# Kernel optimization log

Measured on AMD Instinct MI355X. Metric: run time of the kernel, lower is better.

Reference implementation:

```python
import jax, jax.numpy as jnp
from jax import lax
import numpy as np

IN, HID, NCLS, B, S = 360, 64, 5, 64, 128
MH_CONST = 2.0 / (np.sqrt(3.0) * np.pi ** 0.25)


def setup_inputs() -> dict:
    key = jax.random.key(0)
    ks = jax.random.split(key, 24)
    g = lambda i, shape, s=0.05: jax.random.normal(ks[i], shape, jnp.float32) * s
    inp = {
        'x_seq': jax.random.normal(ks[0], (B, S, IN), jnp.float32),
        # WavKANLinear params (out=64, in=360)
        'wav_scale': jnp.ones((HID, IN), jnp.float32),
        'wav_translation': jnp.zeros((HID, IN), jnp.float32),
        'wav_weights': g(1, (HID, IN)),
        'base_weight': g(2, (HID, IN)),
        # BatchNorm1d (eval mode, running stats)
        'bn_gamma': jnp.ones((HID,), jnp.float32),
        'bn_beta': jnp.zeros((HID,), jnp.float32),
        'bn_mean': jnp.zeros((HID,), jnp.float32),
        'bn_var': jnp.ones((HID,), jnp.float32),
        # LayerNorm(64)
        'ln_gamma': jnp.ones((HID,), jnp.float32),
        'ln_beta': jnp.zeros((HID,), jnp.float32),
        # bidirectional GRU, 1 layer, hidden=64
        'gru_w_ih_f': g(3, (3 * HID, HID)), 'gru_w_hh_f': g(4, (3 * HID, HID)),
        'gru_b_ih_f': g(5, (3 * HID,)), 'gru_b_hh_f': g(6, (3 * HID,)),
        'gru_w_ih_b': g(7, (3 * HID, HID)), 'gru_w_hh_b': g(8, (3 * HID, HID)),
        'gru_b_ih_b': g(9, (3 * HID,)), 'gru_b_hh_b': g(10, (3 * HID,)),
        # classifier: Linear(128,64) -> ReLU -> Linear(64,5)
        'fc1_w': g(11, (HID, 2 * HID)), 'fc1_b': jnp.zeros((HID,), jnp.float32),
        'fc2_w': g(12, (NCLS, HID)), 'fc2_b': jnp.zeros((NCLS,), jnp.float32),
    }
    return inp


def _gru_dir(x_sbf, w_ih, w_hh, b_ih, b_hh, reverse):
    # x_sbf: (S, B, F). Returns final hidden (B, H). PyTorch GRU equations.
    Bn = x_sbf.shape[1]
    H = w_hh.shape[1]
    gi_all = jnp.einsum('sbf,gf->sbg', x_sbf, w_ih) + b_ih  # precompute input gates

    def step(h, gi):
        gh = h @ w_hh.T + b_hh
        i_r, i_z, i_n = jnp.split(gi, 3, axis=-1)
        h_r, h_z, h_n = jnp.split(gh, 3, axis=-1)
        r = jax.nn.sigmoid(i_r + h_r)
        z = jax.nn.sigmoid(i_z + h_z)
        n = jnp.tanh(i_n + r * h_n)
        h_new = (1.0 - z) * n + z * h
        return h_new, None

    h0 = jnp.zeros((Bn, H), x_sbf.dtype)
    h_final, _ = lax.scan(step, h0, gi_all, reverse=reverse)
    return h_final


def reference(x_seq, wav_scale, wav_translation, wav_weights, base_weight,
              bn_gamma, bn_beta, bn_mean, bn_var, ln_gamma, ln_beta,
              gru_w_ih_f, gru_w_hh_f, gru_b_ih_f, gru_b_hh_f,
              gru_w_ih_b, gru_w_hh_b, gru_b_ih_b, gru_b_hh_b,
              fc1_w, fc1_b, fc2_w, fc2_b):
    b, s, f = x_seq.shape
    x_flat = x_seq.reshape(b * s, f)  # (N, 360)

    # --- WavKANLinear (mexican_hat) ---
    x_scaled = (x_flat[:, None, :] - wav_translation[None]) / wav_scale[None]  # (N, 64, 360)
    wavelet = MH_CONST * (x_scaled * x_scaled - 1.0) * jnp.exp(-0.5 * x_scaled * x_scaled)
    wav_out = jnp.einsum('noi,oi->no', wavelet, wav_weights)  # (N, 64)
    base_out = jax.nn.silu(x_flat) @ base_weight.T
    combined = wav_out + base_out
    # BatchNorm1d eval mode
    x_emb = (combined - bn_mean) * lax.rsqrt(bn_var + 1e-5) * bn_gamma + bn_beta

    # --- LayerNorm(64) ---
    mu = jnp.mean(x_emb, axis=-1, keepdims=True)
    var = jnp.mean(jnp.square(x_emb - mu), axis=-1, keepdims=True)
    x_emb = (x_emb - mu) * lax.rsqrt(var + 1e-5) * ln_gamma + ln_beta
    # dropout is identity in eval mode

    x_sbf = x_emb.reshape(b, s, HID).swapaxes(0, 1)  # (S, B, 64)

    # --- bidirectional GRU, take final hiddens ---
    h_fwd = _gru_dir(x_sbf, gru_w_ih_f, gru_w_hh_f, gru_b_ih_f, gru_b_hh_f, False)
    h_bwd = _gru_dir(x_sbf, gru_w_ih_b, gru_w_hh_b, gru_b_ih_b, gru_b_hh_b, True)
    hidden_cat = jnp.concatenate([h_fwd, h_bwd], axis=1)  # (B, 128)

    # --- classifier ---
    h = jax.nn.relu(hidden_cat @ fc1_w.T + fc1_b)
    logits = h @ fc2_w.T + fc2_b
    return logits
```

## Files before the change

### kernel.cpp

```cpp
#include <hip/hip_runtime.h>

#define IN_F   360
#define HIDN   64
#define NCLS   5
#define BATCH  64
#define SEQ    128
#define NROWS  (BATCH*SEQ)

#define WS_FLAG  0
#define WS_WPACK 16
#define WS_WFAST 92176
#define WS_WT4   138256
#define WS_XEMB  162832
#define WS_GI    687120
#define WS_HC    3832848

#define LOG2E        1.4426950408889634f
#define NEG_HALF_L2E (-0.7213475204444817f)

__device__ __forceinline__ float fast_rcp(float x) { return __builtin_amdgcn_rcpf(x); }
__device__ __forceinline__ float fast_rsq(float x) { return __builtin_amdgcn_rsqf(x); }
__device__ __forceinline__ float sigmoid_(float x) {
    x = fminf(fmaxf(x, -60.0f), 60.0f);
    return fast_rcp(1.0f + exp2f(-LOG2E * x));
}
__device__ __forceinline__ float tanh_(float x) {
    x = fminf(fmaxf(x, -30.0f), 30.0f);
    float e = exp2f(-2.8853900817779268f * x);
    return (1.0f - e) * fast_rcp(1.0f + e);
}
__device__ __forceinline__ float readlane_f(float v, int l) {
    return __int_as_float(__builtin_amdgcn_readlane(__float_as_int(v), l));
}

__global__ __launch_bounds__(256) void prep_kernel(
    const float* __restrict__ scale, const float* __restrict__ trans,
    const float* __restrict__ ww,    const float* __restrict__ bw,
    const float* __restrict__ wihf,  const float* __restrict__ wihb,
    float* __restrict__ ws) {
    int idx = blockIdx.x * 256 + threadIdx.x;
    float4* wpack  = (float4*)(ws + WS_WPACK);
    float2* wfast2 = (float2*)(ws + WS_WFAST);
    float*  wT4    = ws + WS_WT4;
    int*    flagp  = (int*)(ws + WS_FLAG);
    if (idx < 64 * IN_F) {
        int o = idx & 63, i = idx >> 6;
        float s  = scale[o * IN_F + i];
        float tr = trans[o * IN_F + i];
        if (s != 1.0f || tr != 0.0f) atomicOr(flagp, 1);
        float a  = 1.0f / s;
        float b  = -tr * a;
        float wq = 0.8673250705840776f * ww[o * IN_F + i];
        float bb = bw[o * IN_F + i];
        wpack[i * 64 + o] = make_float4(a, b, wq, bb);
        wfast2[(i >> 1) * 128 + o * 2 + (i & 1)] = make_float2(wq, bb);
    }
    int idx2 = idx - 64 * IN_F;
    if (idx2 >= 0 && idx2 < 24576) {
        int e = idx2 & 3; int rest = idx2 >> 2;
        int g = rest % 384; int k4 = rest / 384;
        int k = k4 * 4 + e; int dir = g / 192; int gg = g - dir * 192;
        const float* src = dir ? wihb : wihf;
        wT4[idx2] = src[gg * 64 + k];
    }
}

__global__ __launch_bounds__(512) void wavgi_kernel(
    const float* __restrict__ x_seq,
    const float* __restrict__ bn_g, const float* __restrict__ bn_b,
    const float* __restrict__ bn_m, const float* __restrict__ bn_v,
    const float* __restrict__ ln_g, const float* __restrict__ ln_b,
    const float* __restrict__ ws_c,
    const float* __restrict__ bihf, const float* __restrict__ bihb,
    float* __restrict__ gi) {
    __shared__ float2 xs_lds[16 * IN_F];
    __shared__ __align__(16) float xs2[32 * 64];
    int t = threadIdx.x;
    int row0 = blockIdx.x * 32;
    int o = t & 63, grp = t >> 6;
    int fast = (*(const int*)(ws_c + WS_FLAG)) == 0;

    float bscale = bn_g[o] * fast_rsq(bn_v[o] + 1e-5f);
    float bshift = fmaf(-bn_m[o], bscale, bn_b[o]);
    float lg = ln_g[o], lb = ln_b[o];

    for (int st = 0; st < 2; ++st) {
        if (st) __syncthreads();
        float acc0 = 0.f, acc1 = 0.f;
        if (fast) {
            for (int idx = t; idx < 16 * IN_F; idx += 512) {
                int r = idx / IN_F, i = idx - r * IN_F;
                float x = x_seq[(row0 + st * 16 + r) * IN_F + i];
                float u = x * x;
                float phi = (u - 1.0f) * exp2f(u * NEG_HALF_L2E);
                float sl  = x * fast_rcp(1.0f + exp2f(-LOG2E * x));
                xs_lds[idx] = make_float2(phi, sl);
            }
            __syncthreads();
            const float4* wf4 = (const float4*)(ws_c + WS_WFAST);
            const float4* xs4 = (const float4*)xs_lds;
            const float4* xr0 = xs4 + (grp * 2 + 0) * 180;
            const float4* xr1 = xs4 + (grp * 2 + 1) * 180;
            #pragma unroll 2
            for (int i2 = 0; i2 < 180; ++i2) {
                float4 wp = wf4[i2 * 64 + o];
                float4 a = xr0[i2];
                acc0 = fmaf(a.x, wp.x, acc0); acc0 = fmaf(a.y, wp.y, acc0);
                acc0 = fmaf(a.z, wp.z, acc0); acc0 = fmaf(a.w, wp.w, acc0);
                float4 b = xr1[i2];
                acc1 = fmaf(b.x, wp.x, acc1); acc1 = fmaf(b.y, wp.y, acc1);
                acc1 = fmaf(b.z, wp.z, acc1); acc1 = fmaf(b.w, wp.w, acc1);
            }
        } else {
            for (int idx = t; idx < 16 * IN_F; idx += 512) {
                int r = idx / IN_F, i = idx - r * IN_F;
                float x = x_seq[(row0 + st * 16 + r) * IN_F + i];
                float sl = x * fast_rcp(1.0f + exp2f(-LOG2E * x));
                xs_lds[idx] = make_float2(x, sl);
            }
            __syncthreads();
            const float4* wpack = (const float4*)(ws_c + WS_WPACK);
            const float2* xr0 = xs_lds + (grp * 2 + 0) * IN_F;
            const float2* xr1 = xs_lds + (grp * 2 + 1) * IN_F;
            for (int i = 0; i < IN_F; ++i) {
                float4 wp = wpack[i * 64 + o];
                {
                    float2 xs = xr0[i];
                    float xsc = fmaf(xs.x, wp.x, wp.y); float u = xsc * xsc;
                    float e = exp2f(u * NEG_HALF_L2E);
                    acc0 = fmaf((u - 1.0f) * e, wp.z, acc0);
                    acc0 = fmaf(xs.y, wp.w, acc0);
                }
                {
                    float2 xs = xr1[i];
                    float xsc = fmaf(xs.x, wp.x, wp.y); float u = xsc * xsc;
                    float e = exp2f(u * NEG_HALF_L2E);
                    acc1 = fmaf((u - 1.0f) * e, wp.z, acc1);
                    acc1 = fmaf(xs.y, wp.w, acc1);
                }
            }
        }
        float vals[2] = {acc0, acc1};
        #pragma unroll
        for (int rr = 0; rr < 2; ++rr) {
            float y = fmaf(vals[rr], bscale, bshift);
            float s = y;
            #pragma unroll
            for (int m = 1; m < 64; m <<= 1) s += __shfl_xor(s, m, 64);
            float mu = s * (1.0f / 64.0f);
            float d = y - mu;
            float s2 = d * d;
            #pragma unroll
            for (int m = 1; m < 64; m <<= 1) s2 += __shfl_xor(s2, m, 64);
            float rstd = fast_rsq(s2 * (1.0f / 64.0f) + 1e-5f);
            xs2[(st * 16 + grp * 2 + rr) * 64 + o] = fmaf(d * rstd, lg, lb);
        }
    }
    __syncthreads();

    if (t < 384) {
        const float4* wT4 = (const float4*)(ws_c + WS_WT4);
        int dir = t / 192, gg = t - dir * 192;
        float bih = dir ? bihb[gg] : bihf[gg];
        float4 w[16];
        #pragma unroll
        for (int k4 = 0; k4 < 16; ++k4) w[k4] = wT4[k4 * 384 + t];
        for (int r = 0; r < 32; r += 2) {
            const float4* x0 = (const float4*)(xs2 + r * 64);
            const float4* x1 = (const float4*)(xs2 + r * 64 + 64);
            float a0 = bih, a1 = 0.f, b0 = bih, b1 = 0.f;
            #pragma unroll
            for (int k4 = 0; k4 < 16; k4 += 2) {
                float4 xv = x0[k4];     float4 wv = w[k4];
                a0 = fmaf(xv.x, wv.x, a0); a0 = fmaf(xv.y, wv.y, a0);
                a0 = fmaf(xv.z, wv.z, a0); a0 = fmaf(xv.w, wv.w, a0);
                float4 xu = x0[k4 + 1]; float4 wu = w[k4 + 1];
                a1 = fmaf(xu.x, wu.x, a1); a1 = fmaf(xu.y, wu.y, a1);
                a1 = fmaf(xu.z, wu.z, a1); a1 = fmaf(xu.w, wu.w, a1);
                float4 yv = x1[k4];
                b0 = fmaf(yv.x, wv.x, b0); b0 = fmaf(yv.y, wv.y, b0);
                b0 = fmaf(yv.z, wv.z, b0); b0 = fmaf(yv.w, wv.w, b0);
                float4 yu = x1[k4 + 1];
                b1 = fmaf(yu.x, wu.x, b1); b1 = fmaf(yu.y, wu.y, b1);
                b1 = fmaf(yu.z, wu.z, b1); b1 = fmaf(yu.w, wu.w, b1);
            }
            gi[(row0 + r) * 384 + t]     = a0 + a1;
            gi[(row0 + r + 1) * 384 + t] = b0 + b1;
        }
    }
}

__global__ __launch_bounds__(192, 1) void gru_kernel(
    const float* __restrict__ ws_c,
    const float* __restrict__ whhf, const float* __restrict__ bhhf,
    const float* __restrict__ whhb, const float* __restrict__ bhhb,
    float* __restrict__ hc) {
    __shared__ __align__(16) float gi_l[64 * 192];
    __shared__ __align__(16) float ex[2][192];
    const float* gi = ws_c + WS_GI;
    int t = threadIdx.x, lane = t & 63, g = t >> 6;
    int b = blockIdx.x & 63, dir = blockIdx.x >> 6;
    const float* whh = dir ? whhb : whhf;
    const float* bhh = dir ? bhhb : bhhf;

    float w[64];
    {
        const float4* wrow = (const float4*)(whh + t * 64);
        #pragma unroll
        for (int q = 0; q < 16; ++q) {
            float4 a = wrow[q];
            w[4*q] = a.x; w[4*q+1] = a.y; w[4*q+2] = a.z; w[4*q+3] = a.w;
        }
    }
    float bias = bhh[t];

    const float* gsrc = gi + (size_t)(b * SEQ) * 384 + dir * 192 + t;
#define GOFF(s) ((dir ? (SEQ - 1 - (s)) : (s)) * 384)
    #pragma unroll 8
    for (int q = 0; q < 64; ++q) gi_l[q * 192 + t] = gsrc[GOFF(q)];
    float h = 0.0f;
    __syncthreads();

    for (int ss = 0; ss < SEQ; ++ss) {
        if (ss == 64) {
            __syncthreads();
            #pragma unroll 8
            for (int q = 0; q < 64; ++q) gi_l[q * 192 + t] = gsrc[GOFF(64 + q)];
            __syncthreads();
        }
        int ssl = ss & 63, p = ss & 1;
        float giv = gi_l[ssl * 192 + t];
        float inv = gi_l[ssl * 192 + 128 + lane];
        float acc0 = bias, acc1 = 0.f;
        #pragma unroll
        for (int c = 0; c < 4; ++c) {
            float sh[16];
            #pragma unroll
            for (int j = 0; j < 16; ++j) sh[j] = readlane_f(h, c * 16 + j);
            #pragma unroll
            for (int j = 0; j < 16; j += 2) {
                acc0 = fmaf(w[c * 16 + j],     sh[j],     acc0);
                acc1 = fmaf(w[c * 16 + j + 1], sh[j + 1], acc1);
            }
        }
        float a = acc0 + acc1;
        float v = (g == 2) ? a : sigmoid_(giv + a);
        ex[p][t] = v;
        __syncthreads();
        float r   = ex[p][lane];
        float z   = ex[p][64 + lane];
        float an  = ex[p][128 + lane];
        float n = tanh_(fmaf(r, an, inv));
        h = fmaf(z, h - n, n);
    }
#undef GOFF
    if (g == 0) hc[b * 128 + dir * 64 + lane] = h;
}

__global__ __launch_bounds__(64) void head_kernel(
    const float* __restrict__ ws_c,
    const float* __restrict__ fc1w, const float* __restrict__ fc1b,
    const float* __restrict__ fc2w, const float* __restrict__ fc2b,
    float* __restrict__ out) {
    __shared__ __align__(16) float hr[128];
    __shared__ float h1[64];
    const float* hc = ws_c + WS_HC;
    int bb = blockIdx.x, t = threadIdx.x;
    hr[t]      = hc[bb * 128 + t];
    hr[64 + t] = hc[bb * 128 + 64 + t];
    __syncthreads();
    float acc = fc1b[t];
    const float4* w4 = (const float4*)(fc1w + t * 128);
    const float4* h4 = (const float4*)hr;
    #pragma unroll 8
    for (int k4 = 0; k4 < 32; ++k4) {
        float4 wv = w4[k4]; float4 hv = h4[k4];
        acc = fmaf(hv.x, wv.x, acc); acc = fmaf(hv.y, wv.y, acc);
        acc = fmaf(hv.z, wv.z, acc); acc = fmaf(hv.w, wv.w, acc);
    }
    h1[t] = fmaxf(acc, 0.0f);
    __syncthreads();
    if (t < NCLS) {
        float acc2 = fc2b[t];
        const float* wr = fc2w + t * 64;
        #pragma unroll 8
        for (int k = 0; k < 64; ++k) acc2 = fmaf(h1[k], wr[k], acc2);
        out[bb * NCLS + t] = acc2;
    }
}

extern "C" void kernel_launch(void* const* d_in, const int* in_sizes, int n_in,
                              void* d_out, int out_size, void* d_ws, size_t ws_size,
                              hipStream_t stream) {
    const float* x_seq = (const float*)d_in[0];
    const float* wscal = (const float*)d_in[1];
    const float* wtran = (const float*)d_in[2];
    const float* wwght = (const float*)d_in[3];
    const float* bwght = (const float*)d_in[4];
    const float* bn_g  = (const float*)d_in[5];
    const float* bn_b  = (const float*)d_in[6];
    const float* bn_m  = (const float*)d_in[7];
    const float* bn_v  = (const float*)d_in[8];
    const float* ln_g  = (const float*)d_in[9];
    const float* ln_b  = (const float*)d_in[10];
    const float* wihf  = (const float*)d_in[11];
    const float* whhf  = (const float*)d_in[12];
    const float* bihf  = (const float*)d_in[13];
    const float* bhhf  = (const float*)d_in[14];
    const float* wihb  = (const float*)d_in[15];
    const float* whhb  = (const float*)d_in[16];
    const float* bihb  = (const float*)d_in[17];
    const float* bhhb  = (const float*)d_in[18];
    const float* fc1w  = (const float*)d_in[19];
    const float* fc1b  = (const float*)d_in[20];
    const float* fc2w  = (const float*)d_in[21];
    const float* fc2b  = (const float*)d_in[22];
    float* ws  = (float*)d_ws;
    float* out = (float*)d_out;

    hipMemsetAsync(ws + WS_FLAG, 0, sizeof(int), stream);
    hipLaunchKernelGGL(prep_kernel, dim3(186), dim3(256), 0, stream,
                       wscal, wtran, wwght, bwght, wihf, wihb, ws);
    hipLaunchKernelGGL(wavgi_kernel, dim3(NROWS / 32), dim3(512), 0, stream,
                       x_seq, bn_g, bn_b, bn_m, bn_v, ln_g, ln_b, ws,
                       bihf, bihb, ws + WS_GI);
    hipLaunchKernelGGL(gru_kernel, dim3(128), dim3(192), 0, stream,
                       ws, whhf, bhhf, whhb, bhhb, ws + WS_HC);
    hipLaunchKernelGGL(head_kernel, dim3(64), dim3(64), 0, stream,
                       ws, fc1w, fc1b, fc2w, fc2b, out);
}
```

Before: 240.8 us.

## Fuse all stages into one cooperative kernel with grid syncs

Merges the prep, wavelet/gate-precompute, GRU recurrence and classifier-head kernels into a single cooperative launch of 256 blocks, separated by grid-wide barriers. A shared-memory union is reused across stages. The input-gate GEMM loop is also restructured to stream weights once while keeping 32 row accumulators in registers. The aim is to remove per-launch overhead between the four kernels. In exchange, the GRU stage now runs with 512-thread blocks at one block per CU where only 192 threads are active, grid.sync has its own cost, and register pressure rises.

```diff
diff --git a/kernel.cpp b/kernel.cpp
--- a/kernel.cpp
+++ b/kernel.cpp
@@ -1,4 +1,7 @@
 #include <hip/hip_runtime.h>
+#include <hip/hip_cooperative_groups.h>
+
+namespace cg = cooperative_groups;
 
 #define IN_F   360
 #define HIDN   64
@@ -33,259 +36,268 @@
     return __int_as_float(__builtin_amdgcn_readlane(__float_as_int(v), l));
 }
 
-__global__ __launch_bounds__(256) void prep_kernel(
+__global__ __launch_bounds__(512, 1) void mega_kernel(
+    const float* __restrict__ x_seq,
     const float* __restrict__ scale, const float* __restrict__ trans,
     const float* __restrict__ ww,    const float* __restrict__ bw,
+    const float* __restrict__ bn_g,  const float* __restrict__ bn_b,
+    const float* __restrict__ bn_m,  const float* __restrict__ bn_v,
+    const float* __restrict__ ln_g,  const float* __restrict__ ln_b,
     const float* __restrict__ wihf,  const float* __restrict__ wihb,
-    float* __restrict__ ws) {
-    int idx = blockIdx.x * 256 + threadIdx.x;
-    float4* wpack  = (float4*)(ws + WS_WPACK);
-    float2* wfast2 = (float2*)(ws + WS_WFAST);
-    float*  wT4    = ws + WS_WT4;
-    int*    flagp  = (int*)(ws + WS_FLAG);
-    if (idx < 64 * IN_F) {
-        int o = idx & 63, i = idx >> 6;
-        float s  = scale[o * IN_F + i];
-        float tr = trans[o * IN_F + i];
-        if (s != 1.0f || tr != 0.0f) atomicOr(flagp, 1);
-        float a  = 1.0f / s;
-        float b  = -tr * a;
-        float wq = 0.8673250705840776f * ww[o * IN_F + i];
-        float bb = bw[o * IN_F + i];
-        wpack[i * 64 + o] = make_float4(a, b, wq, bb);
-        wfast2[(i >> 1) * 128 + o * 2 + (i & 1)] = make_float2(wq, bb);
+    const float* __restrict__ bihf,  const float* __restrict__ bihb,
+    const float* __restrict__ whhf,  const float* __restrict__ bhhf,
+    const float* __restrict__ whhb,  const float* __restrict__ bhhb,
+    const float* __restrict__ fc1w,  const float* __restrict__ fc1b,
+    const float* __restrict__ fc2w,  const float* __restrict__ fc2b,
+    float* __restrict__ ws, float* __restrict__ out) {
+
+    __shared__ __align__(16) union SM {
+        struct { float2 xs[16 * IN_F]; float xs2[32 * 64]; } s12;
+        struct { float gi_l[64 * 192]; float ex[2][192]; } s3;
+        struct { float hr[128]; float h1[64]; } s4;
+    } sm;
+
+    cg::grid_group grid = cg::this_grid();
+    int t = threadIdx.x, bid = blockIdx.x;
+    float* gi = ws + WS_GI;
+    float* hc = ws + WS_HC;
+
+    {
+        int idx = bid * 512 + t;
+        float4* wpack  = (float4*)(ws + WS_WPACK);
+        float2* wfast2 = (float2*)(ws + WS_WFAST);
+        float*  wT4    = ws + WS_WT4;
+        int*    flagp  = (int*)(ws + WS_FLAG);
+        if (idx < 64 * IN_F) {
+            int o = idx & 63, i = idx >> 6;
+            float s  = scale[o * IN_F + i];
+            float tr = trans[o * IN_F + i];
+            if (s != 1.0f || tr != 0.0f) atomicOr(flagp, 1);
+            float a  = 1.0f / s;
+            float b  = -tr * a;
+            float wq = 0.8673250705840776f * ww[o * IN_F + i];
+            float bb = bw[o * IN_F + i];
+            wpack[i * 64 + o] = make_float4(a, b, wq, bb);
+            wfast2[(i >> 1) * 128 + o * 2 + (i & 1)] = make_float2(wq, bb);
+        }
+        int idx2 = idx - 64 * IN_F;
+        if (idx2 >= 0 && idx2 < 24576) {
+            int e = idx2 & 3; int rest = idx2 >> 2;
+            int g = rest % 384; int k4 = rest / 384;
+            int k = k4 * 4 + e; int dir = g / 192; int gg = g - dir * 192;
+            const float* src = dir ? wihb : wihf;
+            wT4[idx2] = src[gg * 64 + k];
+        }
     }
-    int idx2 = idx - 64 * IN_F;
-    if (idx2 >= 0 && idx2 < 24576) {
-        int e = idx2 & 3; int rest = idx2 >> 2;
-        int g = rest % 384; int k4 = rest / 384;
-        int k = k4 * 4 + e; int dir = g / 192; int gg = g - dir * 192;
-        const float* src = dir ? wihb : wihf;
-        wT4[idx2] = src[gg * 64 + k];
+    __threadfence();
+    grid.sync();
+    __threadfence();
+
+    {
+        int row0 = bid * 32;
+        int o = t & 63, grp = t >> 6;
+        int fast = (*(const int*)(ws + WS_FLAG)) == 0;
+        float bscale = bn_g[o] * fast_rsq(bn_v[o] + 1e-5f);
+        float bshift = fmaf(-bn_m[o], bscale, bn_b[o]);
+        float lg = ln_g[o], lb = ln_b[o];
+
+        for (int st = 0; st < 2; ++st) {
+            if (st) __syncthreads();
+            float acc0 = 0.f, acc1 = 0.f;
+            if (fast) {
+                for (int idx = t; idx < 16 * IN_F; idx += 512) {
+                    int r = idx / IN_F, i = idx - r * IN_F;
+                    float x = x_seq[(row0 + st * 16 + r) * IN_F + i];
+                    float u = x * x;
+                    float phi = (u - 1.0f) * exp2f(u * NEG_HALF_L2E);
+                    float sl  = x * fast_rcp(1.0f + exp2f(-LOG2E * x));
+                    sm.s12.xs[idx] = make_float2(phi, sl);
+                }
+                __syncthreads();
+                const float4* wf4 = (const float4*)(ws + WS_WFAST);
+                const float4* xs4 = (const float4*)sm.s12.xs;
+                const float4* xr0 = xs4 + (grp * 2 + 0) * 180;
+                const float4* xr1 = xs4 + (grp * 2 + 1) * 180;
+                #pragma unroll 2
+                for (int i2 = 0; i2 < 180; ++i2) {
+                    float4 wp = wf4[i2 * 64 + o];
+                    float4 a = xr0[i2];
+                    acc0 = fmaf(a.x, wp.x, acc0); acc0 = fmaf(a.y, wp.y, acc0);
+                    acc0 = fmaf(a.z, wp.z, acc0); acc0 = fmaf(a.w, wp.w, acc0);
+                    float4 b = xr1[i2];
+                    acc1 = fmaf(b.x, wp.x, acc1); acc1 = fmaf(b.y, wp.y, acc1);
+                    acc1 = fmaf(b.z, wp.z, acc1); acc1 = fmaf(b.w, wp.w, acc1);
+                }
+            } else {
+                for (int idx = t; idx < 16 * IN_F; idx += 512) {
+                    int r = idx / IN_F, i = idx - r * IN_F;
+                    float x = x_seq[(row0 + st * 16 + r) * IN_F + i];
+                    float sl = x * fast_rcp(1.0f + exp2f(-LOG2E * x));
+                    sm.s12.xs[idx] = make_float2(x, sl);
+                }
+                __syncthreads();
+                const float4* wpack = (const float4*)(ws + WS_WPACK);
+                const float2* xr0 = sm.s12.xs + (grp * 2 + 0) * IN_F;
+                const float2* xr1 = sm.s12.xs + (grp * 2 + 1) * IN_F;
+                for (int i = 0; i < IN_F; ++i) {
+                    float4 wp = wpack[i * 64 + o];
+                    {
+                        float2 xsv = xr0[i];
+                        float xsc = fmaf(xsv.x, wp.x, wp.y); float u = xsc * xsc;
+                        float e = exp2f(u * NEG_HALF_L2E);
+                        acc0 = fmaf((u - 1.0f) * e, wp.z, acc0);
+                        acc0 = fmaf(xsv.y, wp.w, acc0);
+                    }
+                    {
+                        float2 xsv = xr1[i];
+                        float xsc = fmaf(xsv.x, wp.x, wp.y); float u = xsc * xsc;
+                        float e = exp2f(u * NEG_HALF_L2E);
+                        acc1 = fmaf((u - 1.0f) * e, wp.z, acc1);
+                        acc1 = fmaf(xsv.y, wp.w, acc1);
+                    }
+                }
+            }
+            float vals[2] = {acc0, acc1};
+            #pragma unroll
+            for (int rr = 0; rr < 2; ++rr) {
+                float y = fmaf(vals[rr], bscale, bshift);
+                float s = y;
+                #pragma unroll
+                for (int m = 1; m < 64; m <<= 1) s += __shfl_xor(s, m, 64);
+                float mu = s * (1.0f / 64.0f);
+                float d = y - mu;
+                float s2 = d * d;
+                #pragma unroll
+                for (int m = 1; m < 64; m <<= 1) s2 += __shfl_xor(s2, m, 64);
+                float rstd = fast_rsq(s2 * (1.0f / 64.0f) + 1e-5f);
+                sm.s12.xs2[(st * 16 + grp * 2 + rr) * 64 + o] = fmaf(d * rstd, lg, lb);
+            }
+        }
+        __syncthreads();
+
+        if (t < 384) {
+            const float4* wT4 = (const float4*)(ws + WS_WT4);
+            int dir = t / 192, gg = t - dir * 192;
+            float bih = dir ? bihb[gg] : bihf[gg];
+            float acc[32];
+            #pragma unroll
+            for (int j = 0; j < 32; ++j) acc[j] = bih;
+            const float4* x4 = (const float4*)sm.s12.xs2;
+            for (int k4 = 0; k4 < 16; ++k4) {
+                float4 wv = wT4[k4 * 384 + t];
+                #pragma unroll
+                for (int j = 0; j < 32; ++j) {
+                    float4 xv = x4[j * 16 + k4];
+                    acc[j] = fmaf(xv.x, wv.x, acc[j]);
+                    acc[j] = fmaf(xv.y, wv.y, acc[j]);
+                    acc[j] = fmaf(xv.z, wv.z, acc[j]);
+                    acc[j] = fmaf(xv.w, wv.w, acc[j]);
+                }
+            }
+            #pragma unroll
+            for (int j = 0; j < 32; ++j) gi[(size_t)(row0 + j) * 384 + t] = acc[j];
+        }
     }
-}
-
-__global__ __launch_bounds__(512) void wavgi_kernel(
-    const float* __restrict__ x_seq,
-    const float* __restrict__ bn_g, const float* __restrict__ bn_b,
-    const float* __restrict__ bn_m, const float* __restrict__ bn_v,
-    const float* __restrict__ ln_g, const float* __restrict__ ln_b,
-    const float* __restrict__ ws_c,
-    const float* __restrict__ bihf, const float* __restrict__ bihb,
-    float* __restrict__ gi) {
-    __shared__ float2 xs_lds[16 * IN_F];
-    __shared__ __align__(16) float xs2[32 * 64];
-    int t = threadIdx.x;
-    int row0 = blockIdx.x * 32;
-    int o = t & 63, grp = t >> 6;
-    int fast = (*(const int*)(ws_c + WS_FLAG)) == 0;
-
-    float bscale = bn_g[o] * fast_rsq(bn_v[o] + 1e-5f);
-    float bshift = fmaf(-bn_m[o], bscale, bn_b[o]);
-    float lg = ln_g[o], lb = ln_b[o];
-
-    for (int st = 0; st < 2; ++st) {
-        if (st) __syncthreads();
-        float acc0 = 0.f, acc1 = 0.f;
-        if (fast) {
-            for (int idx = t; idx < 16 * IN_F; idx += 512) {
-                int r = idx / IN_F, i = idx - r * IN_F;
-                float x = x_seq[(row0 + st * 16 + r) * IN_F + i];
-                float u = x * x;
-                float phi = (u - 1.0f) * exp2f(u * NEG_HALF_L2E);
-                float sl  = x * fast_rcp(1.0f + exp2f(-LOG2E * x));
-                xs_lds[idx] = make_float2(phi, sl);
+    __threadfence();
+    grid.sync();
+    __threadfence();
+
+    if (bid < 128) {
+        int lane = t & 63, g = t >> 6;
+        bool act = t < 192;
+        int b = bid & 63, dirg = bid >> 6;
+        const float* whh = dirg ? whhb : whhf;
+        const float* bhh = dirg ? bhhb : bhhf;
+        float w[64];
+        float bias = 0.f, h = 0.f;
+        const float* gsrc = gi + (size_t)(b * SEQ) * 384 + dirg * 192 + t;
+#define GOFF(s) ((dirg ? (SEQ - 1 - (s)) : (s)) * 384)
+        if (act) {
+            const float4* wrow = (const float4*)(whh + t * 64);
+            #pragma unroll
+            for (int q = 0; q < 16; ++q) {
+                float4 a = wrow[q];
+                w[4*q] = a.x; w[4*q+1] = a.y; w[4*q+2] = a.z; w[4*q+3] = a.w;
+            }
+            bias = bhh[t];
+            #pragma unroll 8
+            for (int q = 0; q < 64; ++q) sm.s3.gi_l[q * 192 + t] = gsrc[GOFF(q)];
+        }
+        __syncthreads();
+
+        for (int ss = 0; ss < SEQ; ++ss) {
+            if (ss == 64) {
+                __syncthreads();
+                if (act) {
+                    #pragma unroll 8
+                    for (int q = 0; q < 64; ++q)
+                        sm.s3.gi_l[q * 192 + t] = gsrc[GOFF(64 + q)];
+                }
+                __syncthreads();
+            }
+            int ssl = ss & 63, p = ss & 1;
+            float inv = 0.f;
+            if (act) {
+                float giv = sm.s3.gi_l[ssl * 192 + t];
+                inv       = sm.s3.gi_l[ssl * 192 + 128 + lane];
+                float acc0 = bias, acc1 = 0.f;
+                #pragma unroll
+                for (int c = 0; c < 4; ++c) {
+                    float sh[16];
+                    #pragma unroll
+                    for (int j = 0; j < 16; ++j) sh[j] = readlane_f(h, c * 16 + j);
+                    #pragma unroll
+                    for (int j = 0; j < 16; j += 2) {
+                        acc0 = fmaf(w[c * 16 + j],     sh[j],     acc0);
+                        acc1 = fmaf(w[c * 16 + j + 1], sh[j + 1], acc1);
+                    }
+                }
+                float a = acc0 + acc1;
+                float v = (g == 2) ? a : sigmoid_(giv + a);
+                sm.s3.ex[p][t] = v;
             }
             __syncthreads();
-            const float4* wf4 = (const float4*)(ws_c + WS_WFAST);
-            const float4* xs4 = (const float4*)xs_lds;
-            const float4* xr0 = xs4 + (grp * 2 + 0) * 180;
-            const float4* xr1 = xs4 + (grp * 2 + 1) * 180;
-            #pragma unroll 2
-            for (int i2 = 0; i2 < 180; ++i2) {
-                float4 wp = wf4[i2 * 64 + o];
-                float4 a = xr0[i2];
-                acc0 = fmaf(a.x, wp.x, acc0); acc0 = fmaf(a.y, wp.y, acc0);
-                acc0 = fmaf(a.z, wp.z, acc0); acc0 = fmaf(a.w, wp.w, acc0);
-                float4 b = xr1[i2];
-                acc1 = fmaf(b.x, wp.x, acc1); acc1 = fmaf(b.y, wp.y, acc1);
-                acc1 = fmaf(b.z, wp.z, acc1); acc1 = fmaf(b.w, wp.w, acc1);
-            }
-        } else {
-            for (int idx = t; idx < 16 * IN_F; idx += 512) {
-                int r = idx / IN_F, i = idx - r * IN_F;
-                float x = x_seq[(row0 + st * 16 + r) * IN_F + i];
-                float sl = x * fast_rcp(1.0f + exp2f(-LOG2E * x));
-                xs_lds[idx] = make_float2(x, sl);
-            }
-            __syncthreads();
-            const float4* wpack = (const float4*)(ws_c + WS_WPACK);
-            const float2* xr0 = xs_lds + (grp * 2 + 0) * IN_F;
-            const float2* xr1 = xs_lds + (grp * 2 + 1) * IN_F;
-            for (int i = 0; i < IN_F; ++i) {
-                float4 wp = wpack[i * 64 + o];
-                {
-                    float2 xs = xr0[i];
-                    float xsc = fmaf(xs.x, wp.x, wp.y); float u = xsc * xsc;
-                    float e = exp2f(u * NEG_HALF_L2E);
-                    acc0 = fmaf((u - 1.0f) * e, wp.z, acc0);
-                    acc0 = fmaf(xs.y, wp.w, acc0);
-                }
-                {
-                    float2 xs = xr1[i];
-                    float xsc = fmaf(xs.x, wp.x, wp.y); float u = xsc * xsc;
-                    float e = exp2f(u * NEG_HALF_L2E);
-                    acc1 = fmaf((u - 1.0f) * e, wp.z, acc1);
-                    acc1 = fmaf(xs.y, wp.w, acc1);
-                }
-            }
-        }
-        float vals[2] = {acc0, acc1};
-        #pragma unroll
-        for (int rr = 0; rr < 2; ++rr) {
-            float y = fmaf(vals[rr], bscale, bshift);
-            float s = y;
-            #pragma unroll
-            for (int m = 1; m < 64; m <<= 1) s += __shfl_xor(s, m, 64);
-            float mu = s * (1.0f / 64.0f);
-            float d = y - mu;
-            float s2 = d * d;
-            #pragma unroll
-            for (int m = 1; m < 64; m <<= 1) s2 += __shfl_xor(s2, m, 64);
-            float rstd = fast_rsq(s2 * (1.0f / 64.0f) + 1e-5f);
-            xs2[(st * 16 + grp * 2 + rr) * 64 + o] = fmaf(d * rstd, lg, lb);
-        }
+            if (act) {
+                float r  = sm.s3.ex[p][lane];
+                float z  = sm.s3.ex[p][64 + lane];
+                float an = sm.s3.ex[p][128 + lane];
+                float n = tanh_(fmaf(r, an, inv));
+                h = fmaf(z, h - n, n);
+            }
+        }
+#undef GOFF
+        if (act && g == 0) hc[b * 128 + dirg * 64 + lane] = h;
     }
-    __syncthreads();
-
-    if (t < 384) {
-        const float4* wT4 = (const float4*)(ws_c + WS_WT4);
-        int dir = t / 192, gg = t - dir * 192;
-        float bih = dir ? bihb[gg] : bihf[gg];
-        float4 w[16];
-        #pragma unroll
-        for (int k4 = 0; k4 < 16; ++k4) w[k4] = wT4[k4 * 384 + t];
-        for (int r = 0; r < 32; r += 2) {
-            const float4* x0 = (const float4*)(xs2 + r * 64);
-            const float4* x1 = (const float4*)(xs2 + r * 64 + 64);
-            float a0 = bih, a1 = 0.f, b0 = bih, b1 = 0.f;
-            #pragma unroll
-            for (int k4 = 0; k4 < 16; k4 += 2) {
-                float4 xv = x0[k4];     float4 wv = w[k4];
-                a0 = fmaf(xv.x, wv.x, a0); a0 = fmaf(xv.y, wv.y, a0);
-                a0 = fmaf(xv.z, wv.z, a0); a0 = fmaf(xv.w, wv.w, a0);
-                float4 xu = x0[k4 + 1]; float4 wu = w[k4 + 1];
-                a1 = fmaf(xu.x, wu.x, a1); a1 = fmaf(xu.y, wu.y, a1);
-                a1 = fmaf(xu.z, wu.z, a1); a1 = fmaf(xu.w, wu.w, a1);
-                float4 yv = x1[k4];
-                b0 = fmaf(yv.x, wv.x, b0); b0 = fmaf(yv.y, wv.y, b0);
-                b0 = fmaf(yv.z, wv.z, b0); b0 = fmaf(yv.w, wv.w, b0);
-                float4 yu = x1[k4 + 1];
-                b1 = fmaf(yu.x, wu.x, b1); b1 = fmaf(yu.y, wu.y, b1);
-                b1 = fmaf(yu.z, wu.z, b1); b1 = fmaf(yu.w, wu.w, b1);
-            }
-            gi[(row0 + r) * 384 + t]     = a0 + a1;
-            gi[(row0 + r + 1) * 384 + t] = b0 + b1;
-        }
-    }
-}
-
-__global__ __launch_bounds__(192, 1) void gru_kernel(
-    const float* __restrict__ ws_c,
-    const float* __restrict__ whhf, const float* __restrict__ bhhf,
-    const float* __restrict__ whhb, const float* __restrict__ bhhb,
-    float* __restrict__ hc) {
-    __shared__ __align__(16) float gi_l[64 * 192];
-    __shared__ __align__(16) float ex[2][192];
-    const float* gi = ws_c + WS_GI;
-    int t = threadIdx.x, lane = t & 63, g = t >> 6;
-    int b = blockIdx.x & 63, dir = blockIdx.x >> 6;
-    const float* whh = dir ? whhb : whhf;
-    const float* bhh = dir ? bhhb : bhhf;
-
-    float w[64];
-    {
-        const float4* wrow = (const float4*)(whh + t * 64);
-        #pragma unroll
-        for (int q = 0; q < 16; ++q) {
-            float4 a = wrow[q];
-            w[4*q] = a.x; w[4*q+1] = a.y; w[4*q+2] = a.z; w[4*q+3] = a.w;
-        }
-    }
-    float bias = bhh[t];
-
-    const float* gsrc = gi + (size_t)(b * SEQ) * 384 + dir * 192 + t;
-#define GOFF(s) ((dir ? (SEQ - 1 - (s)) : (s)) * 384)
-    #pragma unroll 8
-    for (int q = 0; q < 64; ++q) gi_l[q * 192 + t] = gsrc[GOFF(q)];
-    float h = 0.0f;
-    __syncthreads();
-
-    for (int ss = 0; ss < SEQ; ++ss) {
-        if (ss == 64) {
-            __syncthreads();
+    __threadfence();
+    grid.sync();
+    __threadfence();
+
+    if (bid < 64) {
+        if (t < 64) {
+            sm.s4.hr[t]      = hc[bid * 128 + t];
+            sm.s4.hr[64 + t] = hc[bid * 128 + 64 + t];
+        }
+        __syncthreads();
+        if (t < 64) {
+            float acc = fc1b[t];
+            const float4* w4 = (const float4*)(fc1w + t * 128);
+            const float4* h4 = (const float4*)sm.s4.hr;
             #pragma unroll 8
-            for (int q = 0; q < 64; ++q) gi_l[q * 192 + t] = gsrc[GOFF(64 + q)];
-            __syncthreads();
-        }
-        int ssl = ss & 63, p = ss & 1;
-        float giv = gi_l[ssl * 192 + t];
-        float inv = gi_l[ssl * 192 + 128 + lane];
-        float acc0 = bias, acc1 = 0.f;
-        #pragma unroll
-        for (int c = 0; c < 4; ++c) {
-            float sh[16];
-            #pragma unroll
-            for (int j = 0; j < 16; ++j) sh[j] = readlane_f(h, c * 16 + j);
-            #pragma unroll
-            for (int j = 0; j < 16; j += 2) {
-                acc0 = fmaf(w[c * 16 + j],     sh[j],     acc0);
-                acc1 = fmaf(w[c * 16 + j + 1], sh[j + 1], acc1);
-            }
-        }
-        float a = acc0 + acc1;
-        float v = (g == 2) ? a : sigmoid_(giv + a);
-        ex[p][t] = v;
+            for (int k4 = 0; k4 < 32; ++k4) {
+                float4 wv = w4[k4]; float4 hv = h4[k4];
+                acc = fmaf(hv.x, wv.x, acc); acc = fmaf(hv.y, wv.y, acc);
+                acc = fmaf(hv.z, wv.z, acc); acc = fmaf(hv.w, wv.w, acc);
+            }
+            sm.s4.h1[t] = fmaxf(acc, 0.0f);
+        }
         __syncthreads();
-        float r   = ex[p][lane];
-        float z   = ex[p][64 + lane];
-        float an  = ex[p][128 + lane];
-        float n = tanh_(fmaf(r, an, inv));
-        h = fmaf(z, h - n, n);
-    }
-#undef GOFF
-    if (g == 0) hc[b * 128 + dir * 64 + lane] = h;
-}
-
-__global__ __launch_bounds__(64) void head_kernel(
-    const float* __restrict__ ws_c,
-    const float* __restrict__ fc1w, const float* __restrict__ fc1b,
-    const float* __restrict__ fc2w, const float* __restrict__ fc2b,
-    float* __restrict__ out) {
-    __shared__ __align__(16) float hr[128];
-    __shared__ float h1[64];
-    const float* hc = ws_c + WS_HC;
-    int bb = blockIdx.x, t = threadIdx.x;
-    hr[t]      = hc[bb * 128 + t];
-    hr[64 + t] = hc[bb * 128 + 64 + t];
-    __syncthreads();
-    float acc = fc1b[t];
-    const float4* w4 = (const float4*)(fc1w + t * 128);
-    const float4* h4 = (const float4*)hr;
-    #pragma unroll 8
-    for (int k4 = 0; k4 < 32; ++k4) {
-        float4 wv = w4[k4]; float4 hv = h4[k4];
-        acc = fmaf(hv.x, wv.x, acc); acc = fmaf(hv.y, wv.y, acc);
-        acc = fmaf(hv.z, wv.z, acc); acc = fmaf(hv.w, wv.w, acc);
-    }
-    h1[t] = fmaxf(acc, 0.0f);
-    __syncthreads();
-    if (t < NCLS) {
-        float acc2 = fc2b[t];
-        const float* wr = fc2w + t * 64;
-        #pragma unroll 8
-        for (int k = 0; k < 64; ++k) acc2 = fmaf(h1[k], wr[k], acc2);
-        out[bb * NCLS + t] = acc2;
+        if (t < NCLS) {
+            float acc2 = fc2b[t];
+            const float* wr = fc2w + t * 64;
+            #pragma unroll 8
+            for (int k = 0; k < 64; ++k) acc2 = fmaf(sm.s4.h1[k], wr[k], acc2);
+            out[bid * NCLS + t] = acc2;
+        }
     }
 }
 
@@ -319,13 +331,15 @@
     float* out = (float*)d_out;
 
     hipMemsetAsync(ws + WS_FLAG, 0, sizeof(int), stream);
-    hipLaunchKernelGGL(prep_kernel, dim3(186), dim3(256), 0, stream,
-                       wscal, wtran, wwght, bwght, wihf, wihb, ws);
-    hipLaunchKernelGGL(wavgi_kernel, dim3(NROWS / 32), dim3(512), 0, stream,
-                       x_seq, bn_g, bn_b, bn_m, bn_v, ln_g, ln_b, ws,
-                       bihf, bihb, ws + WS_GI);
-    hipLaunchKernelGGL(gru_kernel, dim3(128), dim3(192), 0, stream,
-                       ws, whhf, bhhf, whhb, bhhb, ws + WS_HC);
-    hipLaunchKernelGGL(head_kernel, dim3(64), dim3(64), 0, stream,
-                       ws, fc1w, fc1b, fc2w, fc2b, out);
-}
+    void* args[] = {
+        (void*)&x_seq, (void*)&wscal, (void*)&wtran, (void*)&wwght, (void*)&bwght,
+        (void*)&bn_g, (void*)&bn_b, (void*)&bn_m, (void*)&bn_v,
+        (void*)&ln_g, (void*)&ln_b,
+        (void*)&wihf, (void*)&wihb, (void*)&bihf, (void*)&bihb,
+        (void*)&whhf, (void*)&bhhf, (void*)&whhb, (void*)&bhhb,
+        (void*)&fc1w, (void*)&fc1b, (void*)&fc2w, (void*)&fc2b,
+        (void*)&ws, (void*)&out
+    };
+    hipLaunchCooperativeKernel((const void*)mega_kernel, dim3(256), dim3(512),
+                               args, 0, stream);
+}
```

Measured after the change: 581.6 us. 2.42x slower.
